# Kernel optimization log

Measured on AMD Instinct MI355X. Metric: run time of the kernel, lower is better.

## Reference

```python
import jax, jax.numpy as jnp
import numpy as np


def _log_g(x):
    # log of g(x) = where(x>=0, x+0.5, sigmoid(x)), computed stably in log-space
    return jnp.where(x >= 0, jnp.log(jax.nn.relu(x) + 0.5), -jax.nn.softplus(-x))


def _mingru_layer(h, w_hg_l, w_out_l, rms_w_l):
    # h: [B,T,H]; w_hg_l: [2*DI,H]; w_out_l: [H,DI]; rms_w_l: [H]
    hg = jnp.einsum('bth,dh->btd', h, w_hg_l)          # [B,T,2*DI]
    hidden, gate = jnp.split(hg, 2, axis=-1)            # each [B,T,DI]
    log_coeffs = -jax.nn.softplus(gate)                 # log a_t
    log_values = -jax.nn.softplus(-gate) + _log_g(hidden)  # log(z_t * g(h~_t))
    # Heinsen log-space associative scan (prev_hidden = 0, contributes nothing)
    a_star = jnp.cumsum(log_coeffs, axis=1)
    log_h = a_star + jax.lax.cumlogsumexp(log_values - a_star, axis=1)
    out = jnp.exp(log_h)                                # [B,T,DI]
    out = jnp.einsum('btd,hd->bth', out, w_out_l) + h   # proj_out + residual
    eps = jnp.finfo(out.dtype).eps
    out = out * jax.lax.rsqrt(jnp.mean(out * out, axis=-1, keepdims=True) + eps)
    return out * rms_w_l


def setup_inputs() -> dict:
    key = jax.random.key(0)
    ks = jax.random.split(key, 6)
    B, T, OBS, H, DI, L, A = 32, 1024, 512, 512, 1024, 2, 16
    s = 0.05  # weight scale keeps softplus/exp chain well-conditioned
    return {
        'x': jax.random.normal(ks[0], (B, T, OBS), jnp.float32),
        'enc_w': s * jax.random.normal(ks[1], (H, OBS), jnp.float32),
        'enc_b': jnp.zeros((H,), jnp.float32),
        'w_hg': s * jax.random.normal(ks[2], (L, 2 * DI, H), jnp.float32),
        'w_out': s * jax.random.normal(ks[3], (L, H, DI), jnp.float32),
        'rms_w': jnp.ones((L, H), jnp.float32),
        'dec_w': s * jax.random.normal(ks[4], (A, H), jnp.float32),
        'dec_b': jnp.zeros((A,), jnp.float32),
        'val_w': s * jax.random.normal(ks[5], (1, H), jnp.float32),
        'val_b': jnp.zeros((1,), jnp.float32),
    }


def reference(x, enc_w, enc_b, w_hg, w_out, rms_w, dec_w, dec_b, val_w, val_b):
    B, T, _ = x.shape
    # encoder: Linear + exact gelu
    h = jax.nn.gelu(jnp.einsum('bto,ho->bth', x, enc_w) + enc_b, approximate=False)
    for l in range(w_hg.shape[0]):
        h = _mingru_layer(h, w_hg[l], w_out[l], rms_w[l])
    flat = h.reshape(B * T, -1)
    logits = flat @ dec_w.T + dec_b                     # [B*T, A]
    values = (flat @ val_w.T + val_b).reshape(B, T)
    return logits, values
```

## Files before the change

kernel.cpp:

```cpp
#include <hip/hip_runtime.h>
#include <math.h>

#define MROWS 32768
#define T_LEN 1024
#define MT 128

typedef __attribute__((ext_vector_type(8))) short bf16x8;
typedef __attribute__((ext_vector_type(4))) float f32x4;

__device__ __forceinline__ unsigned short f2bf(float f) {
  union { float f; unsigned u; } x; x.f = f;
  unsigned r = x.u + 0x7fffu + ((x.u >> 16) & 1u);
  return (unsigned short)(r >> 16);
}
__device__ __forceinline__ float bf2f(unsigned short u) {
  union { unsigned u; float f; } x; x.u = ((unsigned)u) << 16; return x.f;
}

__device__ __forceinline__ void gload_lds16(const void* g, void* l) {
  __builtin_amdgcn_global_load_lds(
      (const __attribute__((address_space(1))) void*)g,
      (__attribute__((address_space(3))) void*)l, 16, 0, 0);
}

template<int MODE>
__global__ __launch_bounds__(512, 2)
void gemm_bt(const unsigned short* __restrict__ A, int lda,
             const unsigned short* __restrict__ B,
             int N, int K,
             const float* __restrict__ bias,
             const unsigned short* res,
             unsigned short* outb)
{
  __shared__ __align__(16) char smem[131072];
  char* sAb = smem;
  char* sBb = smem + 65536;

  const int tid  = threadIdx.x;
  const int wave = tid >> 6, lane = tid & 63;

  const int nwg = gridDim.x;
  const int lid = blockIdx.x;
  const int swz = (lid & 7) * (nwg >> 3) + (lid >> 3);
  const int m0 = (swz & (MT - 1)) << 8;
  const int n0 = (swz >> 7) << 8;

  const int wm = wave >> 2, wn = wave & 3;
  const int r16 = lane & 15, q = lane >> 4;

  const int srow = lane >> 2;
  const int xl   = (srow & 3) ^ ((srow >> 2) & 3);
  const int cgb  = ((lane & 3) ^ xl) * 16;
  const int rdswz = ((q ^ (r16 & 3) ^ ((r16 >> 2) & 3)) * 16);
  const int aoff = wm * 8192 + r16 * 64 + rdswz;
  const int boff = wn * 4096 + r16 * 64 + rdswz;

  const char* Ab = (const char*)A;
  const char* Bb = (const char*)B;
  const int NT = K >> 5;

  f32x4 acc[8][4];
#pragma unroll
  for (int i = 0; i < 8; i++)
#pragma unroll
    for (int j = 0; j < 4; j++)
#pragma unroll
      for (int e = 0; e < 4; e++) acc[i][j][e] = 0.0f;

  auto stage = [&](int u) {
    const int buf = u & 3;
    const int kt  = u << 5;
    char* dA = sAb + buf * 16384;
    char* dB = sBb + buf * 16384;
#pragma unroll
    for (int i = 0; i < 2; ++i) {
      const int j = wave * 2 + i;
      const int r = j * 16 + srow;
      gload_lds16(Ab + ((size_t)(m0 + r) * lda + kt) * 2 + cgb, dA + j * 1024);
      gload_lds16(Bb + ((size_t)(n0 + r) * K   + kt) * 2 + cgb, dB + j * 1024);
    }
  };

  stage(0); stage(1); stage(2);

  for (int u = 0; u < NT; ++u) {
    if (u + 2 < NT)      asm volatile("s_waitcnt vmcnt(8)" ::: "memory");
    else if (u + 1 < NT) asm volatile("s_waitcnt vmcnt(4)" ::: "memory");
    else                 asm volatile("s_waitcnt vmcnt(0)" ::: "memory");
    __builtin_amdgcn_s_barrier();
    asm volatile("" ::: "memory");

    if (u + 3 < NT) stage(u + 3);

    const char* bufA = sAb + (u & 3) * 16384;
    const char* bufB = sBb + (u & 3) * 16384;
    bf16x8 bfr[4];
#pragma unroll
    for (int nt = 0; nt < 4; ++nt)
      bfr[nt] = *(const bf16x8*)(bufB + boff + nt * 1024);
    __builtin_amdgcn_s_setprio(1);
#pragma unroll
    for (int mt = 0; mt < 8; ++mt) {
      const bf16x8 af = *(const bf16x8*)(bufA + aoff + mt * 1024);
#pragma unroll
      for (int nt = 0; nt < 4; ++nt)
        acc[mt][nt] = __builtin_amdgcn_mfma_f32_16x16x32_bf16(af, bfr[nt], acc[mt][nt], 0, 0, 0);
    }
    __builtin_amdgcn_s_setprio(0);
  }

#pragma unroll
  for (int mt = 0; mt < 8; ++mt) {
#pragma unroll
    for (int nt = 0; nt < 4; ++nt) {
#pragma unroll
      for (int r = 0; r < 4; ++r) {
        const int m = m0 + wm * 128 + mt * 16 + q * 4 + r;
        const int n = n0 + wn * 64 + nt * 16 + r16;
        const size_t idx = (size_t)m * N + n;
        float v = acc[mt][nt][r];
        if (MODE == 0) {
          v += bias[n];
          v = 0.5f * v * (1.0f + erff(v * 0.70710678118654752f));
        } else if (MODE == 2) {
          v += bf2f(res[idx]);
        }
        outb[idx] = f2bf(v);
      }
    }
  }
}

__global__ __launch_bounds__(256)
void scan_kernel(unsigned short* hg) {
  __shared__ unsigned long long sAB[256 * 16];
  __shared__ float sA[16 * 32];
  __shared__ float sH[16 * 32];
  const int b  = blockIdx.x >> 5;
  const int dg = blockIdx.x & 31;
  const int tid = threadIdx.x;
  const int c  = tid >> 4;
  const int dp = tid & 15;
  unsigned int* base = (unsigned int*)(hg + (size_t)b * T_LEN * 2048);
  const int du = dg * 16 + dp;

  float carry = 0.0f;

  for (int seg = 0; seg < 4; ++seg) {
    const int t0 = seg * 256 + c * 16;

    float A0 = 1.0f, A1 = 1.0f, h0 = 0.0f, h1 = 0.0f;
#pragma unroll
    for (int tl = 0; tl < 16; ++tl) {
      const int t = t0 + tl;
      const unsigned hidp = base[t * 1024 + du];
      const unsigned gtp  = base[t * 1024 + 512 + du];
      const float hid0 = bf2f((unsigned short)hidp), hid1 = bf2f((unsigned short)(hidp >> 16));
      const float gt0  = bf2f((unsigned short)gtp),  gt1  = bf2f((unsigned short)(gtp >> 16));
      const float e0 = __expf(-gt0), e1 = __expf(-gt1);
      const float r0 = 1.0f / (1.0f + e0), r1 = 1.0f / (1.0f + e1);
      const float g0 = (hid0 >= 0.0f) ? (hid0 + 0.5f) : (1.0f / (1.0f + __expf(-hid0)));
      const float g1 = (hid1 >= 0.0f) ? (hid1 + 0.5f) : (1.0f / (1.0f + __expf(-hid1)));
      const unsigned short ra0 = f2bf(e0 * r0), rb0 = f2bf(r0 * g0);
      const unsigned short ra1 = f2bf(e1 * r1), rb1 = f2bf(r1 * g1);
      sAB[(c * 16 + tl) * 16 + dp] =
          (unsigned long long)((unsigned)ra0 | ((unsigned)ra1 << 16)) |
          ((unsigned long long)((unsigned)rb0 | ((unsigned)rb1 << 16)) << 32);
      const float fa0 = bf2f(ra0), fb0 = bf2f(rb0), fa1 = bf2f(ra1), fb1 = bf2f(rb1);
      A0 *= fa0; h0 = fa0 * h0 + fb0;
      A1 *= fa1; h1 = fa1 * h1 + fb1;
    }
    sA[c * 32 + 2 * dp] = A0;  sA[c * 32 + 2 * dp + 1] = A1;
    sH[c * 32 + 2 * dp] = h0;  sH[c * 32 + 2 * dp + 1] = h1;
    __syncthreads();

    if (tid < 32) {
      float hin = carry;
#pragma unroll
      for (int cc = 0; cc < 16; ++cc) {
        const float a  = sA[cc * 32 + tid];
        const float hs = sH[cc * 32 + tid];
        sA[cc * 32 + tid] = hin;
        hin = hs + a * hin;
      }
      carry = hin;
    }
    __syncthreads();

    float hh0 = sA[c * 32 + 2 * dp];
    float hh1 = sA[c * 32 + 2 * dp + 1];
#pragma unroll
    for (int tl = 0; tl < 16; ++tl) {
      const int t = t0 + tl;
      const unsigned long long ab = sAB[(c * 16 + tl) * 16 + dp];
      const float fa0 = bf2f((unsigned short)ab);
      const float fa1 = bf2f((unsigned short)(ab >> 16));
      const float fb0 = bf2f((unsigned short)(ab >> 32));
      const float fb1 = bf2f((unsigned short)(ab >> 48));
      hh0 = fa0 * hh0 + fb0;
      hh1 = fa1 * hh1 + fb1;
      base[t * 1024 + 512 + du] = (unsigned)f2bf(hh0) | ((unsigned)f2bf(hh1) << 16);
    }
    __syncthreads();
  }
}

__global__ __launch_bounds__(256)
void rms_kernel(unsigned short* __restrict__ hb, const float* __restrict__ w) {
  const int wid  = (blockIdx.x * blockDim.x + threadIdx.x) >> 6;
  const int lane = threadIdx.x & 63;
  unsigned short* row = hb + (size_t)wid * 512;
  float v[8];
  float ss = 0.0f;
#pragma unroll
  for (int j = 0; j < 8; j++) { v[j] = bf2f(row[lane + 64 * j]); ss += v[j] * v[j]; }
#pragma unroll
  for (int off = 32; off >= 1; off >>= 1) ss += __shfl_xor(ss, off, 64);
  const float r = rsqrtf(ss * (1.0f / 512.0f) + 1.1920929e-7f);
#pragma unroll
  for (int j = 0; j < 8; j++) {
    const int k = lane + 64 * j;
    row[k] = f2bf(v[j] * r * w[k]);
  }
}

__global__ __launch_bounds__(256)
void decoder_kernel(const unsigned short* __restrict__ hb,
                    const float* __restrict__ dec_w,
                    const float* __restrict__ dec_b,
                    const float* __restrict__ val_w,
                    const float* __restrict__ val_b,
                    float* __restrict__ out) {
  const int nw   = (gridDim.x * blockDim.x) >> 6;
  const int wid  = (blockIdx.x * blockDim.x + threadIdx.x) >> 6;
  const int lane = threadIdx.x & 63;
  float* logits = out;
  float* values = out + (size_t)MROWS * 16;
  for (int row = wid; row < MROWS; row += nw) {
    const unsigned short* hr = hb + (size_t)row * 512;
    float acc[17];
#pragma unroll
    for (int a = 0; a < 17; a++) acc[a] = 0.0f;
#pragma unroll
    for (int j = 0; j < 8; j++) {
      const int k = lane + 64 * j;
      const float hv = bf2f(hr[k]);
#pragma unroll
      for (int a = 0; a < 16; a++) acc[a] += hv * dec_w[a * 512 + k];
      acc[16] += hv * val_w[k];
    }
#pragma unroll
    for (int a = 0; a < 17; a++) {
#pragma unroll
      for (int off = 32; off >= 1; off >>= 1) acc[a] += __shfl_xor(acc[a], off, 64);
    }
    if (lane == 0) {
#pragma unroll
      for (int a = 0; a < 16; a++) logits[(size_t)row * 16 + a] = acc[a] + dec_b[a];
      values[row] = acc[16] + val_b[0];
    }
  }
}

__global__ __launch_bounds__(256)
void conv_bf16(const float* __restrict__ in, unsigned short* __restrict__ out, int n4) {
  const int i = blockIdx.x * blockDim.x + threadIdx.x;
  if (i < n4) {
    const float4 v = ((const float4*)in)[i];
    const unsigned long long pack =
        (unsigned long long)f2bf(v.x) |
        ((unsigned long long)f2bf(v.y) << 16) |
        ((unsigned long long)f2bf(v.z) << 32) |
        ((unsigned long long)f2bf(v.w) << 48);
    ((unsigned long long*)out)[i] = pack;
  }
}

extern "C" void kernel_launch(void* const* d_in, const int* in_sizes, int n_in,
                              void* d_out, int out_size, void* d_ws, size_t ws_size,
                              hipStream_t stream) {
  const float* x     = (const float*)d_in[0];
  const float* enc_w = (const float*)d_in[1];
  const float* enc_b = (const float*)d_in[2];
  const float* w_hg  = (const float*)d_in[3];
  const float* w_out = (const float*)d_in[4];
  const float* rms_w = (const float*)d_in[5];
  const float* dec_w = (const float*)d_in[6];
  const float* dec_b = (const float*)d_in[7];
  const float* val_w = (const float*)d_in[8];
  const float* val_b = (const float*)d_in[9];
  float* out = (float*)d_out;

  if (ws_size < 174587904u) return;

  char* ws = (char*)d_ws;
  unsigned short* hg   = (unsigned short*)(ws);
  unsigned short* xb   = (unsigned short*)(ws);
  unsigned short* hb   = (unsigned short*)(ws + 134217728);
  unsigned short* wenc = (unsigned short*)(ws + 167772160);
  unsigned short* whg  = wenc + 262144;
  unsigned short* wout = whg + 2097152;

  conv_bf16<<<16384, 256, 0, stream>>>(x, xb, 4194304);
  conv_bf16<<<256,   256, 0, stream>>>(enc_w, wenc, 65536);
  conv_bf16<<<2048,  256, 0, stream>>>(w_hg, whg, 524288);
  conv_bf16<<<1024,  256, 0, stream>>>(w_out, wout, 262144);

  gemm_bt<0><<<256, 512, 0, stream>>>(xb, 512, wenc, 512, 512, enc_b, nullptr, hb);

  for (int l = 0; l < 2; ++l) {
    gemm_bt<1><<<1024, 512, 0, stream>>>(hb, 512, whg + (size_t)l * 1048576, 2048, 512,
                                         nullptr, nullptr, hg);
    scan_kernel<<<1024, 256, 0, stream>>>(hg);
    gemm_bt<2><<<256, 512, 0, stream>>>(hg + 1024, 2048, wout + (size_t)l * 524288,
                                        512, 1024, nullptr, hb, hb);
    rms_kernel<<<8192, 256, 0, stream>>>(hb, rms_w + (size_t)l * 512);
  }

  decoder_kernel<<<512, 256, 0, stream>>>(hb, dec_w, dec_b, val_w, val_b, out);
}
```

Measured before the change: 680.5 us.

## Switch GEMM to BK=64 double-buffered LDS pipeline with N-major tile order

New measurement: 769.6 us. 13.1% more time.

```diff
diff --git a/kernel.cpp b/kernel.cpp
--- a/kernel.cpp
+++ b/kernel.cpp
@@ -3,7 +3,6 @@
 
 #define MROWS 32768
 #define T_LEN 1024
-#define MT 128
 
 typedef __attribute__((ext_vector_type(8))) short bf16x8;
 typedef __attribute__((ext_vector_type(4))) float f32x4;
@@ -42,22 +41,24 @@
   const int nwg = gridDim.x;
   const int lid = blockIdx.x;
   const int swz = (lid & 7) * (nwg >> 3) + (lid >> 3);
-  const int m0 = (swz & (MT - 1)) << 8;
-  const int n0 = (swz >> 7) << 8;
+  const int ntile = N >> 8;
+  const int m0 = (swz / ntile) << 8;
+  const int n0 = (swz % ntile) << 8;
 
   const int wm = wave >> 2, wn = wave & 3;
   const int r16 = lane & 15, q = lane >> 4;
 
-  const int srow = lane >> 2;
-  const int xl   = (srow & 3) ^ ((srow >> 2) & 3);
-  const int cgb  = ((lane & 3) ^ xl) * 16;
-  const int rdswz = ((q ^ (r16 & 3) ^ ((r16 >> 2) & 3)) * 16);
-  const int aoff = wm * 8192 + r16 * 64 + rdswz;
-  const int boff = wn * 4096 + r16 * 64 + rdswz;
+  const int srow   = lane >> 3;
+  const int sslotb = ((lane & 7) ^ srow) * 16;
+
+  const int slot0 = (q ^ (r16 & 7)) * 16;
+  const int slot1 = ((4 | q) ^ (r16 & 7)) * 16;
+  const int ra = (wm * 128 + r16) * 128;
+  const int rb = (wn * 64  + r16) * 128;
 
   const char* Ab = (const char*)A;
   const char* Bb = (const char*)B;
-  const int NT = K >> 5;
+  const int NT = K >> 6;
 
   f32x4 acc[8][4];
 #pragma unroll
@@ -68,45 +69,54 @@
       for (int e = 0; e < 4; e++) acc[i][j][e] = 0.0f;
 
   auto stage = [&](int u) {
-    const int buf = u & 3;
-    const int kt  = u << 5;
-    char* dA = sAb + buf * 16384;
-    char* dB = sBb + buf * 16384;
-#pragma unroll
-    for (int i = 0; i < 2; ++i) {
-      const int j = wave * 2 + i;
-      const int r = j * 16 + srow;
-      gload_lds16(Ab + ((size_t)(m0 + r) * lda + kt) * 2 + cgb, dA + j * 1024);
-      gload_lds16(Bb + ((size_t)(n0 + r) * K   + kt) * 2 + cgb, dB + j * 1024);
+    const int kt = u << 6;
+    char* dA = sAb + (u & 1) * 32768;
+    char* dB = sBb + (u & 1) * 32768;
+#pragma unroll
+    for (int i = 0; i < 4; ++i) {
+      const int j = wave * 4 + i;
+      const int r = j * 8 + srow;
+      gload_lds16(Ab + ((size_t)(m0 + r) * lda + kt) * 2 + sslotb, dA + j * 1024);
+      gload_lds16(Bb + ((size_t)(n0 + r) * K   + kt) * 2 + sslotb, dB + j * 1024);
     }
   };
 
-  stage(0); stage(1); stage(2);
+  stage(0);
 
   for (int u = 0; u < NT; ++u) {
-    if (u + 2 < NT)      asm volatile("s_waitcnt vmcnt(8)" ::: "memory");
-    else if (u + 1 < NT) asm volatile("s_waitcnt vmcnt(4)" ::: "memory");
-    else                 asm volatile("s_waitcnt vmcnt(0)" ::: "memory");
-    __builtin_amdgcn_s_barrier();
-    asm volatile("" ::: "memory");
-
-    if (u + 3 < NT) stage(u + 3);
-
-    const char* bufA = sAb + (u & 3) * 16384;
-    const char* bufB = sBb + (u & 3) * 16384;
-    bf16x8 bfr[4];
-#pragma unroll
-    for (int nt = 0; nt < 4; ++nt)
-      bfr[nt] = *(const bf16x8*)(bufB + boff + nt * 1024);
-    __builtin_amdgcn_s_setprio(1);
-#pragma unroll
-    for (int mt = 0; mt < 8; ++mt) {
-      const bf16x8 af = *(const bf16x8*)(bufA + aoff + mt * 1024);
-#pragma unroll
-      for (int nt = 0; nt < 4; ++nt)
-        acc[mt][nt] = __builtin_amdgcn_mfma_f32_16x16x32_bf16(af, bfr[nt], acc[mt][nt], 0, 0, 0);
-    }
-    __builtin_amdgcn_s_setprio(0);
+    __syncthreads();
+    if (u + 1 < NT) stage(u + 1);
+
+    const char* bA = sAb + (u & 1) * 32768;
+    const char* bB = sBb + (u & 1) * 32768;
+
+    bf16x8 bfr[4][2];
+#pragma unroll
+    for (int nt = 0; nt < 4; ++nt) {
+      bfr[nt][0] = *(const bf16x8*)(bB + rb + nt * 2048 + slot0);
+      bfr[nt][1] = *(const bf16x8*)(bB + rb + nt * 2048 + slot1);
+    }
+#pragma unroll
+    for (int qd = 0; qd < 4; ++qd) {
+      bf16x8 af[2][2];
+#pragma unroll
+      for (int i = 0; i < 2; ++i) {
+        const int mt = qd * 2 + i;
+        af[i][0] = *(const bf16x8*)(bA + ra + mt * 2048 + slot0);
+        af[i][1] = *(const bf16x8*)(bA + ra + mt * 2048 + slot1);
+      }
+      __builtin_amdgcn_s_setprio(1);
+#pragma unroll
+      for (int i = 0; i < 2; ++i)
+#pragma unroll
+        for (int nt = 0; nt < 4; ++nt) {
+          acc[qd * 2 + i][nt] = __builtin_amdgcn_mfma_f32_16x16x32_bf16(
+              af[i][0], bfr[nt][0], acc[qd * 2 + i][nt], 0, 0, 0);
+          acc[qd * 2 + i][nt] = __builtin_amdgcn_mfma_f32_16x16x32_bf16(
+              af[i][1], bfr[nt][1], acc[qd * 2 + i][nt], 0, 0, 0);
+        }
+      __builtin_amdgcn_s_setprio(0);
+    }
   }
 
 #pragma unroll
```
